# Kernel tuning notes

Hardware: AMD Instinct MI355X
Metric: run time of the kernel (lower is better)

The kernel has to match this reference:

```python
import jax, jax.numpy as jnp
import numpy as np

NUM_LAYER = 5
NUM_FEATURES = 128
DIM = 256
NUM_BOND_TYPE = 6
NUM_BOND_DIR = 3
BN_EPS = 1e-5


def setup_inputs() -> dict:
    key = jax.random.key(0)
    ks = jax.random.split(key, 16)
    N, E = 100000, 400000
    x = jax.random.normal(ks[0], (N, NUM_FEATURES), dtype=jnp.float32)
    edge_index = jax.random.randint(ks[1], (2, E), 0, N, dtype=jnp.int32)
    edge_attr = jax.random.randint(ks[2], (E, 2), 0, 3, dtype=jnp.int32)
    s = 0.05
    Wl = jax.random.normal(ks[3], (NUM_FEATURES, DIM), dtype=jnp.float32) * s
    bl = jnp.zeros((DIM,), dtype=jnp.float32)
    W1 = jax.random.normal(ks[4], (NUM_LAYER, DIM, 2 * DIM), dtype=jnp.float32) * s
    b1 = jnp.zeros((NUM_LAYER, 2 * DIM), dtype=jnp.float32)
    W2 = jax.random.normal(ks[5], (NUM_LAYER, 2 * DIM, DIM), dtype=jnp.float32) * s
    b2 = jnp.zeros((NUM_LAYER, DIM), dtype=jnp.float32)
    E1 = jax.random.normal(ks[6], (NUM_LAYER, NUM_BOND_TYPE, DIM), dtype=jnp.float32) * s
    E2 = jax.random.normal(ks[7], (NUM_LAYER, NUM_BOND_DIR, DIM), dtype=jnp.float32) * s
    gamma = jnp.ones((NUM_LAYER, DIM), dtype=jnp.float32)
    beta = jnp.zeros((NUM_LAYER, DIM), dtype=jnp.float32)
    return {"x": x, "edge_index": edge_index, "edge_attr": edge_attr,
            "Wl": Wl, "bl": bl, "W1": W1, "b1": b1, "W2": W2, "b2": b2,
            "E1": E1, "E2": E2, "gamma": gamma, "beta": beta}


def reference(x, edge_index, edge_attr, Wl, bl, W1, b1, W2, b2, E1, E2, gamma, beta):
    N = x.shape[0]
    src, dst = edge_index[0], edge_index[1]
    bt, bd = edge_attr[:, 0], edge_attr[:, 1]
    # input projection + activation
    h = jax.nn.relu(x @ Wl + bl)  # [N, D]
    for l in range(NUM_LAYER):
        # edge embeddings (real edges) + self-loop embedding (attr = [4, 0])
        eemb = E1[l][bt] + E2[l][bd]                      # [E, D]
        self_emb = E1[l][4] + E2[l][0]                    # [D]
        msg = h[src] + eemb                               # gather + add
        agg = jax.ops.segment_sum(msg, dst, num_segments=N)
        agg = agg + h + self_emb                          # self-loop messages
        # 2-layer MLP update
        hid = jax.nn.relu(agg @ W1[l] + b1[l])
        out = hid @ W2[l] + b2[l]
        # BatchNorm1d (training mode: batch stats, biased variance)
        mean = jnp.mean(out, axis=0)
        var = jnp.mean((out - mean) ** 2, axis=0)
        h = gamma[l] * (out - mean) * jax.lax.rsqrt(var + BN_EPS) + beta[l]
    # JK = 'last'
    return h
```

## Files before the change

### kernel.cpp

```cpp
#include <hip/hip_runtime.h>
#include <hip/hip_bf16.h>


typedef __bf16 bf16x8 __attribute__((ext_vector_type(8)));
typedef __bf16 bf16x4 __attribute__((ext_vector_type(4)));
typedef float f32x4 __attribute__((ext_vector_type(4)));

#define LDSTRIDE 40

__global__ __launch_bounds__(256, 2)
void gemm0_kernel(const float* __restrict__ Av, const __bf16* __restrict__ BT,
                  const float* __restrict__ bias, float* __restrict__ Cv,
                  int M, int K, int Nc)
{
    __shared__ __bf16 As[128 * LDSTRIDE];
    __shared__ __bf16 Bs[128 * LDSTRIDE];

    const int tid  = threadIdx.x;
    const int wave = tid >> 6;
    const int lane = tid & 63;
    const int quad = lane >> 4;
    const int l16  = lane & 15;
    const int wm   = wave >> 1;
    const int wn   = wave & 1;

    const int col0 = blockIdx.x * 128;
    const int row0 = blockIdx.y * 128;

    f32x4 acc[4][4];
#pragma unroll
    for (int mt = 0; mt < 4; ++mt)
#pragma unroll
        for (int nt = 0; nt < 4; ++nt) acc[mt][nt] = (f32x4){0.f, 0.f, 0.f, 0.f};

    const int srow = tid >> 1;
    const int scol = (tid & 1) * 16;
    const int a_row = row0 + srow;
    const bool a_ok = (a_row < M);
    const __bf16* Bp = BT + (size_t)(col0 + srow) * K + scol;

    for (int k0 = 0; k0 < K; k0 += 32) {
        bf16x8 a0, a1;
        const float* Ap = Av + (size_t)a_row * K + k0 + scol;
        f32x4 x0 = {0,0,0,0}, x1 = {0,0,0,0}, x2 = {0,0,0,0}, x3 = {0,0,0,0};
        if (a_ok) {
            x0 = *(const f32x4*)(Ap);
            x1 = *(const f32x4*)(Ap + 4);
            x2 = *(const f32x4*)(Ap + 8);
            x3 = *(const f32x4*)(Ap + 12);
        }
#pragma unroll
        for (int j = 0; j < 4; ++j) {
            a0[j] = (__bf16)x0[j]; a0[4 + j] = (__bf16)x1[j];
            a1[j] = (__bf16)x2[j]; a1[4 + j] = (__bf16)x3[j];
        }
        bf16x8 b0 = *(const bf16x8*)(Bp + k0);
        bf16x8 b1 = *(const bf16x8*)(Bp + k0 + 8);

        __syncthreads();
        *(bf16x8*)&As[srow * LDSTRIDE + scol]     = a0;
        *(bf16x8*)&As[srow * LDSTRIDE + scol + 8] = a1;
        *(bf16x8*)&Bs[srow * LDSTRIDE + scol]     = b0;
        *(bf16x8*)&Bs[srow * LDSTRIDE + scol + 8] = b1;
        __syncthreads();

        bf16x8 af[4], bfr[4];
#pragma unroll
        for (int mt = 0; mt < 4; ++mt)
            af[mt] = *(const bf16x8*)&As[(wm * 64 + mt * 16 + l16) * LDSTRIDE + quad * 8];
#pragma unroll
        for (int nt = 0; nt < 4; ++nt)
            bfr[nt] = *(const bf16x8*)&Bs[(wn * 64 + nt * 16 + l16) * LDSTRIDE + quad * 8];

#pragma unroll
        for (int mt = 0; mt < 4; ++mt)
#pragma unroll
            for (int nt = 0; nt < 4; ++nt)
                acc[mt][nt] = __builtin_amdgcn_mfma_f32_16x16x32_bf16(
                    af[mt], bfr[nt], acc[mt][nt], 0, 0, 0);
    }

#pragma unroll
    for (int nt = 0; nt < 4; ++nt) {
        const int col = col0 + wn * 64 + nt * 16 + l16;
        const float b = bias[col];
#pragma unroll
        for (int mt = 0; mt < 4; ++mt) {
#pragma unroll
            for (int r = 0; r < 4; ++r) {
                const int row = row0 + wm * 64 + mt * 16 + quad * 4 + r;
                if (row < M) {
                    float v = fmaxf(acc[mt][nt][r] + b, 0.f);
                    Cv[(size_t)row * Nc + col] = v;
                }
            }
        }
    }
}

#define HST 72

__global__ __launch_bounds__(256, 3)
void fused_mlp_kernel(const __bf16* __restrict__ aggb,
                      const __bf16* __restrict__ W1T, const float* __restrict__ b1,
                      const __bf16* __restrict__ W2T, const float* __restrict__ b2,
                      float* __restrict__ out, float* __restrict__ sums, int M)
{
    __shared__ __bf16 As[64 * 256];
    __shared__ __bf16 hidS[2][64 * HST];

    const int tid  = threadIdx.x;
    const int wave = tid >> 6;
    const int lane = tid & 63;
    const int quad = lane >> 4;
    const int l16  = lane & 15;
    const int row0 = blockIdx.x * 64;

    {
        const int srow = tid >> 2;
        const int gb8  = (tid & 3) * 8;
        const int m = row0 + srow;
        bf16x8 v[8];
        if (m < M) {
            const __bf16* Ap = aggb + (size_t)m * 256 + gb8 * 8;
#pragma unroll
            for (int j = 0; j < 8; ++j) v[j] = *(const bf16x8*)(Ap + j * 8);
        } else {
#pragma unroll
            for (int j = 0; j < 8; ++j)
#pragma unroll
                for (int q = 0; q < 8; ++q) v[j][q] = (__bf16)0.f;
        }
#pragma unroll
        for (int j = 0; j < 8; ++j) {
            const int sg = (gb8 + j) ^ (srow & 7);
            *(bf16x8*)&As[srow * 256 + sg * 8] = v[j];
        }
    }

    const int cb = wave * 64;
    f32x4 acc2[4][4];
#pragma unroll
    for (int mt = 0; mt < 4; ++mt)
#pragma unroll
        for (int nt = 0; nt < 4; ++nt) acc2[mt][nt] = (f32x4){0.f, 0.f, 0.f, 0.f};

    const __bf16* W1p = W1T + (size_t)(wave * 16 + l16) * 256 + quad * 8;
    const __bf16* W2p = W2T + (size_t)(cb + l16) * 512 + quad * 8;

#pragma unroll 1
    for (int c = 0; c <= 8; ++c) {
        __syncthreads();

        bf16x8 W1f[8];
        if (c < 8) {
            const __bf16* p = W1p + (size_t)(c * 64) * 256;
#pragma unroll
            for (int kk = 0; kk < 8; ++kk)
                W1f[kk] = *(const bf16x8*)(p + kk * 32);
        }

        if (c >= 1) {
            bf16x8 W2f[4][2];
#pragma unroll
            for (int nt = 0; nt < 4; ++nt)
#pragma unroll
                for (int kkl = 0; kkl < 2; ++kkl)
                    W2f[nt][kkl] = *(const bf16x8*)(W2p + (size_t)(nt * 16) * 512
                                                    + (c - 1) * 64 + kkl * 32);
            const __bf16* buf = hidS[(c - 1) & 1];
#pragma unroll
            for (int kkl = 0; kkl < 2; ++kkl) {
                bf16x8 Hf[4];
#pragma unroll
                for (int mt = 0; mt < 4; ++mt)
                    Hf[mt] = *(const bf16x8*)&buf[(mt * 16 + l16) * HST + kkl * 32 + quad * 8];
#pragma unroll
                for (int mt = 0; mt < 4; ++mt)
#pragma unroll
                    for (int nt = 0; nt < 4; ++nt)
                        acc2[mt][nt] = __builtin_amdgcn_mfma_f32_16x16x32_bf16(
                            Hf[mt], W2f[nt][kkl], acc2[mt][nt], 0, 0, 0);
            }
        }

        if (c < 8) {
            f32x4 acc1[4];
#pragma unroll
            for (int mt = 0; mt < 4; ++mt) acc1[mt] = (f32x4){0.f, 0.f, 0.f, 0.f};
#pragma unroll
            for (int kk = 0; kk < 8; ++kk) {
                const int sg = (kk * 4 + quad) ^ (l16 & 7);
                bf16x8 af[4];
#pragma unroll
                for (int mt = 0; mt < 4; ++mt)
                    af[mt] = *(const bf16x8*)&As[(mt * 16 + l16) * 256 + sg * 8];
#pragma unroll
                for (int mt = 0; mt < 4; ++mt)
                    acc1[mt] = __builtin_amdgcn_mfma_f32_16x16x32_bf16(
                        af[mt], W1f[kk], acc1[mt], 0, 0, 0);
            }
            __bf16* buf = hidS[c & 1];
            const int lcol = wave * 16 + l16;
            const float bb = b1[c * 64 + lcol];
#pragma unroll
            for (int mt = 0; mt < 4; ++mt)
#pragma unroll
                for (int r = 0; r < 4; ++r) {
                    float v = fmaxf(acc1[mt][r] + bb, 0.f);
                    buf[(mt * 16 + quad * 4 + r) * HST + lcol] = (__bf16)v;
                }
        }
    }

    float* srep = sums + (blockIdx.x & 7) * 512;
#pragma unroll
    for (int nt = 0; nt < 4; ++nt) {
        const int col = cb + nt * 16 + l16;
        const float bb = b2[col];
        float s = 0.f, ss = 0.f;
#pragma unroll
        for (int mt = 0; mt < 4; ++mt) {
#pragma unroll
            for (int r = 0; r < 4; ++r) {
                const int row = row0 + mt * 16 + quad * 4 + r;
                if (row < M) {
                    float v = acc2[mt][nt][r] + bb;
                    out[(size_t)row * 256 + col] = v;
                    s += v; ss += v * v;
                }
            }
        }
        s += __shfl_xor(s, 16); ss += __shfl_xor(ss, 16);
        s += __shfl_xor(s, 32); ss += __shfl_xor(ss, 32);
        if (lane < 16) {
            atomicAdd(&srep[col], s);
            atomicAdd(&srep[256 + col], ss);
        }
    }
}

__global__ void convert_wt_kernel(const float* __restrict__ W, __bf16* __restrict__ WT,
                                  int K, int Nc, int total)
{
    int i = blockIdx.x * 256 + threadIdx.x;
    if (i >= total) return;
    int kn = K * Nc;
    int l = i / kn;
    int rem = i - l * kn;
    int n = rem / K;
    int k = rem - n * K;
    WT[i] = (__bf16)W[(size_t)l * kn + (size_t)k * Nc + n];
}


__global__ void zero_counts_kernel(int* __restrict__ counts, int N)
{
    int i = blockIdx.x * 256 + threadIdx.x;
    if (i < N) counts[i] = 0;
}

__global__ void hist_kernel(const int* __restrict__ ei, int* __restrict__ counts, int E)
{
    int e = blockIdx.x * 256 + threadIdx.x;
    if (e < E) atomicAdd(&counts[ei[E + e]], 1);
}

__global__ void scan1_kernel(const int* __restrict__ counts, int* __restrict__ partial,
                             int* __restrict__ blocksums, int N)
{
    __shared__ int sm[256];
    int i = blockIdx.x * 256 + threadIdx.x;
    int v = (i < N) ? counts[i] : 0;
    sm[threadIdx.x] = v;
    __syncthreads();
    for (int off = 1; off < 256; off <<= 1) {
        int t = 0;
        if ((int)threadIdx.x >= off) t = sm[threadIdx.x - off];
        __syncthreads();
        if ((int)threadIdx.x >= off) sm[threadIdx.x] += t;
        __syncthreads();
    }
    if (i < N) partial[i] = sm[threadIdx.x] - v;
    if (threadIdx.x == 255) blocksums[blockIdx.x] = sm[255];
}

__global__ void scan2_kernel(int* __restrict__ blocksums, int NB)
{
    __shared__ int sm[1024];
    int v = ((int)threadIdx.x < NB) ? blocksums[threadIdx.x] : 0;
    sm[threadIdx.x] = v;
    __syncthreads();
    for (int off = 1; off < 1024; off <<= 1) {
        int t = 0;
        if ((int)threadIdx.x >= off) t = sm[threadIdx.x - off];
        __syncthreads();
        if ((int)threadIdx.x >= off) sm[threadIdx.x] += t;
        __syncthreads();
    }
    if ((int)threadIdx.x < NB) blocksums[threadIdx.x] = sm[threadIdx.x] - v;
}

__global__ void scan3_kernel(const int* __restrict__ partial, const int* __restrict__ blocksums,
                             int* __restrict__ rowptr, int* __restrict__ woff, int N, int E)
{
    int i = blockIdx.x * 256 + threadIdx.x;
    if (i < N) {
        int v = partial[i] + blocksums[blockIdx.x];
        rowptr[i] = v;
        woff[i] = v;
    }
    if (i == 0) rowptr[N] = E;
}

__global__ void scatter_sort_kernel(const int* __restrict__ ei, const int* __restrict__ ea,
                                    int* __restrict__ woff, int* __restrict__ sorted, int E)
{
    int e = blockIdx.x * 256 + threadIdx.x;
    if (e >= E) return;
    int dst = ei[E + e];
    int src = ei[e];
    int c = ea[2 * e] * 3 + ea[2 * e + 1];
    int pos = atomicAdd(&woff[dst], 1);
    sorted[pos] = (src << 4) | c;
}


__global__ void build_table_kernel(const float* __restrict__ E1, const float* __restrict__ E2,
                                   int l, float* __restrict__ tab, float* __restrict__ selfemb,
                                   float* __restrict__ sums)
{
    int b = blockIdx.x;
    int t = threadIdx.x;
    const float* e1 = E1 + (size_t)l * 6 * 256;
    const float* e2 = E2 + (size_t)l * 3 * 256;
    if (b < 9) {
        tab[b * 256 + t] = e1[(b / 3) * 256 + t] + e2[(b % 3) * 256 + t];
    } else {
        selfemb[t] = e1[4 * 256 + t] + e2[0 * 256 + t];
#pragma unroll
        for (int r = 0; r < 16; ++r) sums[r * 256 + t] = 0.f;
    }
}

template<int APPLY_BN>
__global__ __launch_bounds__(256)
void gather_kernel(const float* __restrict__ out, const int* __restrict__ rowptr,
                   const int* __restrict__ sorted, const float* __restrict__ tab,
                   const float* __restrict__ selfemb, const float* __restrict__ scsh,
                   __bf16* __restrict__ aggb, int N)
{
    int n = blockIdx.x * 4 + (threadIdx.x >> 6);
    if (n >= N) return;
    int lane = threadIdx.x & 63;
    int f = lane * 4;

    f32x4 sc, sh;
    if (APPLY_BN) {
        sc = *(const f32x4*)(scsh + f);
        sh = *(const f32x4*)(scsh + 256 + f);
    }

    int r0 = rowptr[n];
    int r1 = rowptr[n + 1];

    f32x4 hv = *(const f32x4*)(out + (size_t)n * 256 + f);
    if (APPLY_BN) hv = hv * sc + sh;
    f32x4 acc = hv + *(const f32x4*)(selfemb + f);

    for (int e = r0; e < r1; ++e) {
        int v = sorted[e];
        f32x4 xv = *(const f32x4*)(out + (size_t)(v >> 4) * 256 + f);
        if (APPLY_BN) xv = xv * sc + sh;
        acc += xv + *(const f32x4*)(tab + (v & 15) * 256 + f);
    }
    bf16x4 o;
#pragma unroll
    for (int j = 0; j < 4; ++j) o[j] = (__bf16)acc[j];
    *(bf16x4*)(aggb + (size_t)n * 256 + f) = o;
}

__global__ void bn_finalize_kernel(const float* __restrict__ sums,
                                   const float* __restrict__ gamma,
                                   const float* __restrict__ beta,
                                   int l, int M, float* __restrict__ scsh)
{
    int c = threadIdx.x;
    float s = 0.f, ss = 0.f;
#pragma unroll
    for (int r = 0; r < 8; ++r) {
        s  += sums[r * 512 + c];
        ss += sums[r * 512 + 256 + c];
    }
    float inv = 1.f / (float)M;
    float mean = s * inv;
    float var = ss * inv - mean * mean;
    float sc = gamma[l * 256 + c] * rsqrtf(var + 1e-5f);
    scsh[c] = sc;
    scsh[256 + c] = beta[l * 256 + c] - mean * sc;
}

__global__ __launch_bounds__(256)
void bn_apply_kernel(const float* __restrict__ out, const float* __restrict__ scsh,
                     float* __restrict__ h, int total4)
{
    int i = blockIdx.x * 256 + threadIdx.x;
    if (i >= total4) return;
    int cg = i & 63;
    f32x4 sc = ((const f32x4*)scsh)[cg];
    f32x4 sh = ((const f32x4*)scsh)[64 + cg];
    f32x4 v = ((const f32x4*)out)[i];
    ((f32x4*)h)[i] = v * sc + sh;
}

extern "C" void kernel_launch(void* const* d_in, const int* in_sizes, int n_in,
                              void* d_out, int out_size, void* d_ws, size_t ws_size,
                              hipStream_t stream)
{
    const float* x     = (const float*)d_in[0];
    const int*   ei    = (const int*)d_in[1];
    const int*   ea    = (const int*)d_in[2];
    const float* Wl    = (const float*)d_in[3];
    const float* bl    = (const float*)d_in[4];
    const float* W1    = (const float*)d_in[5];
    const float* b1    = (const float*)d_in[6];
    const float* W2    = (const float*)d_in[7];
    const float* b2    = (const float*)d_in[8];
    const float* E1    = (const float*)d_in[9];
    const float* E2    = (const float*)d_in[10];
    const float* gamma = (const float*)d_in[11];
    const float* beta  = (const float*)d_in[12];

    const int N = in_sizes[0] / 128;
    const int E = in_sizes[1] / 2;

    __bf16* aggb = (__bf16*)d_out;
    float*  hfin = (float*)d_out;

    float*  out  = (float*)d_ws;
    __bf16* WlT  = (__bf16*)(out + (size_t)N * 256);
    __bf16* W1T  = WlT + 256 * 128;
    __bf16* W2T  = W1T + 5 * 512 * 256;
    float*  tab  = (float*)(W2T + 5 * 256 * 512);
    float*  selfemb = tab + 9 * 256;
    float*  sums = selfemb + 256;
    float*  scsh = sums + 4096;
    int*    counts = (int*)(scsh + 512);
    int*    partial = counts + N;
    int*    rowptr  = partial + N;
    int*    woff    = rowptr + N + 1;
    int*    sorted  = woff + N;
    int*    blocksums = sorted + E;

    const int NB = (N + 255) / 256;
    const int EB = (E + 255) / 256;

    zero_counts_kernel<<<NB, 256, 0, stream>>>(counts, N);
    hist_kernel<<<EB, 256, 0, stream>>>(ei, counts, E);
    scan1_kernel<<<NB, 256, 0, stream>>>(counts, partial, blocksums, N);
    scan2_kernel<<<1, 1024, 0, stream>>>(blocksums, NB);
    scan3_kernel<<<NB, 256, 0, stream>>>(partial, blocksums, rowptr, woff, N, E);
    scatter_sort_kernel<<<EB, 256, 0, stream>>>(ei, ea, woff, sorted, E);

    convert_wt_kernel<<<(128 * 256 + 255) / 256, 256, 0, stream>>>(Wl, WlT, 128, 256, 128 * 256);
    convert_wt_kernel<<<(5 * 256 * 512 + 255) / 256, 256, 0, stream>>>(W1, W1T, 256, 512, 5 * 256 * 512);
    convert_wt_kernel<<<(5 * 512 * 256 + 255) / 256, 256, 0, stream>>>(W2, W2T, 512, 256, 5 * 512 * 256);

    const int mtiles128 = (N + 127) / 128;
    const int mtiles64  = (N + 63) / 64;
    const int total4 = N * 64;
    const int ew_blocks = (total4 + 255) / 256;
    const int gb = (N + 3) / 4;

    gemm0_kernel<<<dim3(2, mtiles128), 256, 0, stream>>>(x, WlT, bl, out, N, 128, 256);

    for (int l = 0; l < 5; ++l) {
        build_table_kernel<<<10, 256, 0, stream>>>(E1, E2, l, tab, selfemb, sums);
        if (l == 0)
            gather_kernel<0><<<gb, 256, 0, stream>>>(out, rowptr, sorted, tab, selfemb,
                                                     scsh, aggb, N);
        else
            gather_kernel<1><<<gb, 256, 0, stream>>>(out, rowptr, sorted, tab, selfemb,
                                                     scsh, aggb, N);
        fused_mlp_kernel<<<mtiles64, 256, 0, stream>>>(
            aggb, W1T + (size_t)l * 512 * 256, b1 + l * 512,
            W2T + (size_t)l * 256 * 512, b2 + l * 256, out, sums, N);
        bn_finalize_kernel<<<1, 256, 0, stream>>>(sums, gamma, beta, l, N, scsh);
    }
    bn_apply_kernel<<<ew_blocks, 256, 0, stream>>>(out, scsh, hfin, total4);
}
```

Before: 1.461 ms.

## Restructure fused MLP into two 256-wide hidden halves with interleaved GEMMs

Replaces the 8-chunk, 64-column hidden pipeline with two halves of 256 hidden columns. Each wave now computes a 64x64 tile of the first GEMM, with 16 MFMAs per k-step instead of 4. The first half's second GEMM is interleaved with the second half's first GEMM in one k-loop. This cuts barrier count and improves reuse of the A fragments loaded from LDS. In exchange it doubles accumulator registers and grows the hidden LDS buffer to a full 64x256 XOR-swizzled tile, and it lowers the occupancy hint from 3 to 2 blocks per SIMD.

```diff
diff --git a/kernel.cpp b/kernel.cpp
--- a/kernel.cpp
+++ b/kernel.cpp
@@ -98,16 +98,15 @@
     }
 }
 
-#define HST 72
-
-__global__ __launch_bounds__(256, 3)
+
+__global__ __launch_bounds__(256, 2)
 void fused_mlp_kernel(const __bf16* __restrict__ aggb,
                       const __bf16* __restrict__ W1T, const float* __restrict__ b1,
                       const __bf16* __restrict__ W2T, const float* __restrict__ b2,
                       float* __restrict__ out, float* __restrict__ sums, int M)
 {
     __shared__ __bf16 As[64 * 256];
-    __shared__ __bf16 hidS[2][64 * HST];
+    __shared__ __bf16 hidS[64 * 256];
 
     const int tid  = threadIdx.x;
     const int wave = tid >> 6;
@@ -137,80 +136,137 @@
             *(bf16x8*)&As[srow * 256 + sg * 8] = v[j];
         }
     }
+    __syncthreads();
 
     const int cb = wave * 64;
+    const __bf16* W1p = W1T + (size_t)(cb + l16) * 256 + quad * 8;
+    const __bf16* W2p = W2T + (size_t)(cb + l16) * 512 + quad * 8;
+
     f32x4 acc2[4][4];
 #pragma unroll
     for (int mt = 0; mt < 4; ++mt)
 #pragma unroll
         for (int nt = 0; nt < 4; ++nt) acc2[mt][nt] = (f32x4){0.f, 0.f, 0.f, 0.f};
 
-    const __bf16* W1p = W1T + (size_t)(wave * 16 + l16) * 256 + quad * 8;
-    const __bf16* W2p = W2T + (size_t)(cb + l16) * 512 + quad * 8;
-
-#pragma unroll 1
-    for (int c = 0; c <= 8; ++c) {
-        __syncthreads();
-
-        bf16x8 W1f[8];
-        if (c < 8) {
-            const __bf16* p = W1p + (size_t)(c * 64) * 256;
-#pragma unroll
-            for (int kk = 0; kk < 8; ++kk)
-                W1f[kk] = *(const bf16x8*)(p + kk * 32);
-        }
-
-        if (c >= 1) {
-            bf16x8 W2f[4][2];
+    f32x4 acc1[4][4];
+
+#pragma unroll
+    for (int mt = 0; mt < 4; ++mt)
+#pragma unroll
+        for (int nt = 0; nt < 4; ++nt) acc1[mt][nt] = (f32x4){0.f, 0.f, 0.f, 0.f};
+#pragma unroll
+    for (int kk = 0; kk < 8; ++kk) {
+        bf16x8 W1f[4];
+#pragma unroll
+        for (int nt = 0; nt < 4; ++nt)
+            W1f[nt] = *(const bf16x8*)(W1p + (size_t)(nt * 16) * 256 + kk * 32);
+        const int sg = (kk * 4 + quad) ^ (l16 & 7);
+        bf16x8 af[4];
+#pragma unroll
+        for (int mt = 0; mt < 4; ++mt)
+            af[mt] = *(const bf16x8*)&As[(mt * 16 + l16) * 256 + sg * 8];
+#pragma unroll
+        for (int mt = 0; mt < 4; ++mt)
 #pragma unroll
             for (int nt = 0; nt < 4; ++nt)
-#pragma unroll
-                for (int kkl = 0; kkl < 2; ++kkl)
-                    W2f[nt][kkl] = *(const bf16x8*)(W2p + (size_t)(nt * 16) * 512
-                                                    + (c - 1) * 64 + kkl * 32);
-            const __bf16* buf = hidS[(c - 1) & 1];
-#pragma unroll
-            for (int kkl = 0; kkl < 2; ++kkl) {
-                bf16x8 Hf[4];
-#pragma unroll
-                for (int mt = 0; mt < 4; ++mt)
-                    Hf[mt] = *(const bf16x8*)&buf[(mt * 16 + l16) * HST + kkl * 32 + quad * 8];
-#pragma unroll
-                for (int mt = 0; mt < 4; ++mt)
-#pragma unroll
-                    for (int nt = 0; nt < 4; ++nt)
-                        acc2[mt][nt] = __builtin_amdgcn_mfma_f32_16x16x32_bf16(
-                            Hf[mt], W2f[nt][kkl], acc2[mt][nt], 0, 0, 0);
-            }
-        }
-
-        if (c < 8) {
-            f32x4 acc1[4];
-#pragma unroll
-            for (int mt = 0; mt < 4; ++mt) acc1[mt] = (f32x4){0.f, 0.f, 0.f, 0.f};
-#pragma unroll
-            for (int kk = 0; kk < 8; ++kk) {
-                const int sg = (kk * 4 + quad) ^ (l16 & 7);
-                bf16x8 af[4];
-#pragma unroll
-                for (int mt = 0; mt < 4; ++mt)
-                    af[mt] = *(const bf16x8*)&As[(mt * 16 + l16) * 256 + sg * 8];
-#pragma unroll
-                for (int mt = 0; mt < 4; ++mt)
-                    acc1[mt] = __builtin_amdgcn_mfma_f32_16x16x32_bf16(
-                        af[mt], W1f[kk], acc1[mt], 0, 0, 0);
-            }
-            __bf16* buf = hidS[c & 1];
-            const int lcol = wave * 16 + l16;
-            const float bb = b1[c * 64 + lcol];
+                acc1[mt][nt] = __builtin_amdgcn_mfma_f32_16x16x32_bf16(
+                    af[mt], W1f[nt], acc1[mt][nt], 0, 0, 0);
+    }
+
+    {
+#pragma unroll
+        for (int nt = 0; nt < 4; ++nt) {
+            const int col = cb + nt * 16 + l16;
+            const float bb = b1[col];
+            const int colgrp = col >> 3;
+            const int c7 = col & 7;
 #pragma unroll
             for (int mt = 0; mt < 4; ++mt)
 #pragma unroll
                 for (int r = 0; r < 4; ++r) {
-                    float v = fmaxf(acc1[mt][r] + bb, 0.f);
-                    buf[(mt * 16 + quad * 4 + r) * HST + lcol] = (__bf16)v;
+                    const int row = mt * 16 + quad * 4 + r;
+                    float v = fmaxf(acc1[mt][nt][r] + bb, 0.f);
+                    hidS[row * 256 + ((colgrp ^ (row & 7)) << 3) + c7] = (__bf16)v;
                 }
         }
+    }
+    __syncthreads();
+
+#pragma unroll
+    for (int mt = 0; mt < 4; ++mt)
+#pragma unroll
+        for (int nt = 0; nt < 4; ++nt) acc1[mt][nt] = (f32x4){0.f, 0.f, 0.f, 0.f};
+#pragma unroll
+    for (int kk = 0; kk < 8; ++kk) {
+        bf16x8 W2f[4];
+#pragma unroll
+        for (int nt = 0; nt < 4; ++nt)
+            W2f[nt] = *(const bf16x8*)(W2p + (size_t)(nt * 16) * 512 + kk * 32);
+        const int sg = (kk * 4 + quad) ^ (l16 & 7);
+        bf16x8 Hf[4];
+#pragma unroll
+        for (int mt = 0; mt < 4; ++mt)
+            Hf[mt] = *(const bf16x8*)&hidS[(mt * 16 + l16) * 256 + sg * 8];
+#pragma unroll
+        for (int mt = 0; mt < 4; ++mt)
+#pragma unroll
+            for (int nt = 0; nt < 4; ++nt)
+                acc2[mt][nt] = __builtin_amdgcn_mfma_f32_16x16x32_bf16(
+                    Hf[mt], W2f[nt], acc2[mt][nt], 0, 0, 0);
+
+        bf16x8 W1f[4];
+#pragma unroll
+        for (int nt = 0; nt < 4; ++nt)
+            W1f[nt] = *(const bf16x8*)(W1p + (size_t)(256 + nt * 16) * 256 + kk * 32);
+        bf16x8 af[4];
+#pragma unroll
+        for (int mt = 0; mt < 4; ++mt)
+            af[mt] = *(const bf16x8*)&As[(mt * 16 + l16) * 256 + sg * 8];
+#pragma unroll
+        for (int mt = 0; mt < 4; ++mt)
+#pragma unroll
+            for (int nt = 0; nt < 4; ++nt)
+                acc1[mt][nt] = __builtin_amdgcn_mfma_f32_16x16x32_bf16(
+                    af[mt], W1f[nt], acc1[mt][nt], 0, 0, 0);
+    }
+    __syncthreads();
+
+    {
+#pragma unroll
+        for (int nt = 0; nt < 4; ++nt) {
+            const int col = cb + nt * 16 + l16;
+            const float bb = b1[256 + col];
+            const int colgrp = col >> 3;
+            const int c7 = col & 7;
+#pragma unroll
+            for (int mt = 0; mt < 4; ++mt)
+#pragma unroll
+                for (int r = 0; r < 4; ++r) {
+                    const int row = mt * 16 + quad * 4 + r;
+                    float v = fmaxf(acc1[mt][nt][r] + bb, 0.f);
+                    hidS[row * 256 + ((colgrp ^ (row & 7)) << 3) + c7] = (__bf16)v;
+                }
+        }
+    }
+    __syncthreads();
+
+#pragma unroll
+    for (int kk = 0; kk < 8; ++kk) {
+        bf16x8 W2f[4];
+#pragma unroll
+        for (int nt = 0; nt < 4; ++nt)
+            W2f[nt] = *(const bf16x8*)(W2p + (size_t)(nt * 16) * 512 + 256 + kk * 32);
+        const int sg = (kk * 4 + quad) ^ (l16 & 7);
+        bf16x8 Hf[4];
+#pragma unroll
+        for (int mt = 0; mt < 4; ++mt)
+            Hf[mt] = *(const bf16x8*)&hidS[(mt * 16 + l16) * 256 + sg * 8];
+#pragma unroll
+        for (int mt = 0; mt < 4; ++mt)
+#pragma unroll
+            for (int nt = 0; nt < 4; ++nt)
+                acc2[mt][nt] = __builtin_amdgcn_mfma_f32_16x16x32_bf16(
+                    Hf[mt], W2f[nt], acc2[mt][nt], 0, 0, 0);
     }
 
     float* srep = sums + (blockIdx.x & 7) * 512;
```

New measurement: 1.543 ms. 5.6% more time.

## Single-buffer swizzled hidden tile in fused MLP and unroll aggregation gather by four

Applied to the files above, without the earlier changes.

The fused MLP kernel swaps the padded double-buffered hidden tile for a single XOR-swizzled 64x64 buffer. It loads W1/W2 fragments just in time instead of prefetching whole arrays, which cuts LDS and register use so occupancy can rise to 4 blocks per CU. This adds an extra barrier per chunk. Separately, the aggregation gather loop is unrolled by four so several neighbor row loads are in flight at once, raising memory-level parallelism at the cost of slightly different float summation order.

```diff
diff --git a/kernel.cpp b/kernel.cpp
--- a/kernel.cpp
+++ b/kernel.cpp
@@ -98,16 +98,15 @@
     }
 }
 
-#define HST 72
-
-__global__ __launch_bounds__(256, 3)
+
+__global__ __launch_bounds__(256, 4)
 void fused_mlp_kernel(const __bf16* __restrict__ aggb,
                       const __bf16* __restrict__ W1T, const float* __restrict__ b1,
                       const __bf16* __restrict__ W2T, const float* __restrict__ b2,
                       float* __restrict__ out, float* __restrict__ sums, int M)
 {
     __shared__ __bf16 As[64 * 256];
-    __shared__ __bf16 hidS[2][64 * HST];
+    __shared__ __bf16 hidS[64 * 64];
 
     const int tid  = threadIdx.x;
     const int wave = tid >> 6;
@@ -137,6 +136,7 @@
             *(bf16x8*)&As[srow * 256 + sg * 8] = v[j];
         }
     }
+    __syncthreads();
 
     const int cb = wave * 64;
     f32x4 acc2[4][4];
@@ -150,46 +150,39 @@
 
 #pragma unroll 1
     for (int c = 0; c <= 8; ++c) {
-        __syncthreads();
-
-        bf16x8 W1f[8];
-        if (c < 8) {
-            const __bf16* p = W1p + (size_t)(c * 64) * 256;
-#pragma unroll
-            for (int kk = 0; kk < 8; ++kk)
-                W1f[kk] = *(const bf16x8*)(p + kk * 32);
-        }
-
         if (c >= 1) {
-            bf16x8 W2f[4][2];
-#pragma unroll
-            for (int nt = 0; nt < 4; ++nt)
-#pragma unroll
-                for (int kkl = 0; kkl < 2; ++kkl)
-                    W2f[nt][kkl] = *(const bf16x8*)(W2p + (size_t)(nt * 16) * 512
-                                                    + (c - 1) * 64 + kkl * 32);
-            const __bf16* buf = hidS[(c - 1) & 1];
 #pragma unroll
             for (int kkl = 0; kkl < 2; ++kkl) {
-                bf16x8 Hf[4];
-#pragma unroll
-                for (int mt = 0; mt < 4; ++mt)
-                    Hf[mt] = *(const bf16x8*)&buf[(mt * 16 + l16) * HST + kkl * 32 + quad * 8];
+                bf16x8 W2f[4], Hf[4];
+#pragma unroll
+                for (int nt = 0; nt < 4; ++nt)
+                    W2f[nt] = *(const bf16x8*)(W2p + (size_t)(nt * 16) * 512
+                                               + (c - 1) * 64 + kkl * 32);
+#pragma unroll
+                for (int mt = 0; mt < 4; ++mt) {
+                    const int row = mt * 16 + l16;
+                    const int sg = (kkl * 4 + quad) ^ (row & 7);
+                    Hf[mt] = *(const bf16x8*)&hidS[row * 64 + sg * 8];
+                }
 #pragma unroll
                 for (int mt = 0; mt < 4; ++mt)
 #pragma unroll
                     for (int nt = 0; nt < 4; ++nt)
                         acc2[mt][nt] = __builtin_amdgcn_mfma_f32_16x16x32_bf16(
-                            Hf[mt], W2f[nt][kkl], acc2[mt][nt], 0, 0, 0);
+                            Hf[mt], W2f[nt], acc2[mt][nt], 0, 0, 0);
             }
         }
 
         if (c < 8) {
+            __syncthreads();
+
             f32x4 acc1[4];
 #pragma unroll
             for (int mt = 0; mt < 4; ++mt) acc1[mt] = (f32x4){0.f, 0.f, 0.f, 0.f};
+            const __bf16* p = W1p + (size_t)(c * 64) * 256;
 #pragma unroll
             for (int kk = 0; kk < 8; ++kk) {
+                bf16x8 W1f = *(const bf16x8*)(p + kk * 32);
                 const int sg = (kk * 4 + quad) ^ (l16 & 7);
                 bf16x8 af[4];
 #pragma unroll
@@ -198,18 +191,24 @@
 #pragma unroll
                 for (int mt = 0; mt < 4; ++mt)
                     acc1[mt] = __builtin_amdgcn_mfma_f32_16x16x32_bf16(
-                        af[mt], W1f[kk], acc1[mt], 0, 0, 0);
+                        af[mt], W1f, acc1[mt], 0, 0, 0);
             }
-            __bf16* buf = hidS[c & 1];
-            const int lcol = wave * 16 + l16;
-            const float bb = b1[c * 64 + lcol];
-#pragma unroll
-            for (int mt = 0; mt < 4; ++mt)
-#pragma unroll
-                for (int r = 0; r < 4; ++r) {
-                    float v = fmaxf(acc1[mt][r] + bb, 0.f);
-                    buf[(mt * 16 + quad * 4 + r) * HST + lcol] = (__bf16)v;
-                }
+
+            {
+                const int lcol = wave * 16 + l16;
+                const float bb = b1[c * 64 + lcol];
+                const int colgrp = lcol >> 3;
+                const int c7 = lcol & 7;
+#pragma unroll
+                for (int mt = 0; mt < 4; ++mt)
+#pragma unroll
+                    for (int r = 0; r < 4; ++r) {
+                        const int row = mt * 16 + quad * 4 + r;
+                        float v = fmaxf(acc1[mt][r] + bb, 0.f);
+                        hidS[row * 64 + ((colgrp ^ (row & 7)) << 3) + c7] = (__bf16)v;
+                    }
+            }
+            __syncthreads();
         }
     }
 
@@ -368,7 +367,30 @@
     if (APPLY_BN) hv = hv * sc + sh;
     f32x4 acc = hv + *(const f32x4*)(selfemb + f);
 
-    for (int e = r0; e < r1; ++e) {
+    int e = r0;
+#pragma unroll 1
+    for (; e + 4 <= r1; e += 4) {
+        int v0 = sorted[e + 0];
+        int v1 = sorted[e + 1];
+        int v2 = sorted[e + 2];
+        int v3 = sorted[e + 3];
+        f32x4 x0 = *(const f32x4*)(out + (size_t)(v0 >> 4) * 256 + f);
+        f32x4 x1 = *(const f32x4*)(out + (size_t)(v1 >> 4) * 256 + f);
+        f32x4 x2 = *(const f32x4*)(out + (size_t)(v2 >> 4) * 256 + f);
+        f32x4 x3 = *(const f32x4*)(out + (size_t)(v3 >> 4) * 256 + f);
+        f32x4 t0 = *(const f32x4*)(tab + (v0 & 15) * 256 + f);
+        f32x4 t1 = *(const f32x4*)(tab + (v1 & 15) * 256 + f);
+        f32x4 t2 = *(const f32x4*)(tab + (v2 & 15) * 256 + f);
+        f32x4 t3 = *(const f32x4*)(tab + (v3 & 15) * 256 + f);
+        if (APPLY_BN) {
+            x0 = x0 * sc + sh; x1 = x1 * sc + sh;
+            x2 = x2 * sc + sh; x3 = x3 * sc + sh;
+        }
+        acc += (x0 + t0) + (x1 + t1);
+        acc += (x2 + t2) + (x3 + t3);
+    }
+#pragma unroll 1
+    for (; e < r1; ++e) {
         int v = sorted[e];
         f32x4 xv = *(const f32x4*)(out + (size_t)(v >> 4) * 256 + f);
         if (APPLY_BN) xv = xv * sc + sh;
```

After: 1.436 ms. About the same (-1.7%).
